# Optimization experiments

Measured on AMD Instinct MI355X. Metric: run time of the kernel, lower is better.

## Reference

```python
import jax, jax.numpy as jnp
import numpy as np

B, S, I, H = 128, 1024, 512, 1024


def setup_inputs() -> dict:
    key = jax.random.key(0)
    k0, k1, k2 = jax.random.split(key, 3)
    scale = 0.02
    return {
        "x": jax.random.normal(k0, (B, S, I), jnp.float32),
        "feature_weighting": jnp.ones((1, 1, I), jnp.float32),
        "temporal_weighting": jnp.ones((1, S, 1), jnp.float32),
        "magnitude": jnp.ones((1,), jnp.float32),
        "W0": jax.random.normal(k1, (3 * H, I + H), jnp.float32) * scale,
        "b0": jnp.zeros((3 * H,), jnp.float32),
        "W1": jax.random.normal(k2, (3 * H, 2 * H), jnp.float32) * scale,
        "b1": jnp.zeros((3 * H,), jnp.float32),
    }


def _cell(x_t, h_prev, c_prev, W, b):
    # gates: [B, 3H] from cat(x, h_prev) @ W.T + b
    gates = jnp.concatenate([x_t, h_prev], axis=1) @ W.T + b
    i, g, o = jnp.split(gates, 3, axis=1)
    f = jax.nn.sigmoid(c_prev)            # note: forget gate from c_prev (module's quirk)
    c_new = f * c_prev + jax.nn.sigmoid(i) * jnp.tanh(g)
    h_new = jax.nn.sigmoid(o) * jnp.tanh(c_new) * f  # extra *f (module's quirk)
    return h_new, c_new


def reference(x, feature_weighting, temporal_weighting, magnitude, W0, b0, W1, b1):
    batch = x.shape[0]
    hid = W0.shape[0] // 3
    x = x * feature_weighting * temporal_weighting * jnp.exp(magnitude)
    zeros = jnp.zeros((batch, hid), x.dtype)
    init = (zeros, zeros, zeros, zeros)  # h0, c0, h1, c1

    def step(carry, x_t):
        h0, c0, h1, c1 = carry
        h0, c0 = _cell(x_t, h0, c0, W0, b0)
        h1, c1 = _cell(h0, h1, c1, W1, b1)
        return (h0, c0, h1, c1), h1

    (h0, c0, h1, c1), ys = jax.lax.scan(step, init, jnp.swapaxes(x, 0, 1))
    outputs = jnp.swapaxes(ys, 0, 1)  # [B, S, H]
    return outputs, ((h0, c0), (h1, c1))
```

## Files before the change

kernel.cpp:

```cpp
#include <hip/hip_runtime.h>
#include <hip/hip_bf16.h>


typedef __attribute__((ext_vector_type(8))) _Float16 f16x8;
typedef __attribute__((ext_vector_type(4))) float f32x4;
typedef unsigned long long u64;
#define DEV __device__ __forceinline__

namespace {
constexpr int Bb = 128, Ss = 1024, Ii = 512, Hh = 1024;
constexpr int K0 = Ii + Hh;
constexpr int K1 = 2 * Hh;
constexpr int NWG = 256;
constexpr int NPH = Ss + 1;
constexpr int RING = 16;

constexpr size_t BH    = (size_t)Bb * Hh;
constexpr size_t OF_H0 = (size_t)Bb * Ss * Hh;
constexpr size_t OF_C0 = OF_H0 + BH;
constexpr size_t OF_H1 = OF_C0 + BH;
constexpr size_t OF_C1 = OF_H1 + BH;

constexpr size_t WS_GO    = 0;
constexpr size_t WS_SLOTS = 256;
constexpr size_t WS_C0    = 4096;
constexpr size_t WS_C1    = WS_C0 + BH * 4;
constexpr size_t RINGF    = (size_t)RING * BH * 2;
constexpr size_t WS_H0F   = WS_C1 + BH * 4;
constexpr size_t WS_H1F   = WS_H0F + RINGF;
constexpr size_t WS_ZEND  = WS_H1F + RINGF;
constexpr size_t WSZ_W0   = (size_t)3 * Hh * K0 * 2;
constexpr size_t WSZ_W1   = (size_t)3 * Hh * K1 * 2;
constexpr size_t WS_W0F   = WS_ZEND;
constexpr size_t WS_W1F   = WS_W0F + WSZ_W0;
constexpr size_t WS_NEED  = WS_W1F + WSZ_W1;

constexpr int CHUNKB    = 3072;
constexpr int LO_BYTES  = 48 * CHUNKB;
constexpr int RED_BYTES = 4 * 3 * 64 * 16;
constexpr int DYN_LDS   = LO_BYTES + RED_BYTES;
}

DEV unsigned short f16b(float f) {
  return __builtin_bit_cast(unsigned short, (_Float16)f);
}
DEV float sig_(float x) { return 1.f / (1.f + __expf(-x)); }
DEV float tanh_(float x) {
  float e = __expf(-2.f * fabsf(x));
  return copysignf((1.f - e) / (1.f + e), x);
}
DEV f16x8 ldh(const unsigned short* p) { return *reinterpret_cast<const f16x8*>(p); }
#define MFMAH __builtin_amdgcn_mfma_f32_16x16x32_f16

__global__ void k_zero(uint4* p, int n16) {
  for (int i = blockIdx.x * blockDim.x + threadIdx.x; i < n16; i += gridDim.x * blockDim.x)
    p[i] = make_uint4(0u, 0u, 0u, 0u);
}

__global__ void k_convert(const float* __restrict__ W0, const float* __restrict__ W1,
                          unsigned short* __restrict__ w0f, unsigned short* __restrict__ w1f) {
  const long NW04 = (long)3 * Hh * K0 / 4;
  const long NW14 = (long)3 * Hh * K1 / 4;
  const long total = NW04 + NW14;
  for (long i = (long)blockIdx.x * blockDim.x + threadIdx.x; i < total;
       i += (long)gridDim.x * blockDim.x) {
    long e; const float* src; unsigned short* dst;
    if (i < NW04) { e = i * 4;          src = W0 + e; dst = w0f + e; }
    else          { e = (i - NW04) * 4; src = W1 + e; dst = w1f + e; }
    f32x4 v = *(const f32x4*)src;
    u64 pk = 0;
#pragma unroll
    for (int e2 = 0; e2 < 4; ++e2) pk |= (u64)f16b(v[e2]) << (16 * e2);
    *(u64*)dst = pk;
  }
}

#define LD_W(g, kl)                                                           \
  (*(const f16x8*)(lds + ((kl) >> 5) * CHUNKB + (g) * 1024 + l4 * 256 + l15 * 16))

#define BLOCK8_L(hP, kaB, koB)                                                \
  do {                                                                        \
    f16x8 aH[8];                                                              \
    _Pragma("unroll") for (int c8 = 0; c8 < 8; ++c8)                          \
      aH[c8] = ldh((hP) + (kaB) + c8 * 32);                                   \
    _Pragma("unroll") for (int c8 = 0; c8 < 8; ++c8) {                        \
      const int ko_ = (koB) + c8 * 32;                                        \
      f32x4 &I = (c8 & 1) ? aI1 : aI0;                                        \
      f32x4 &G = (c8 & 1) ? aG1 : aG0;                                        \
      f32x4 &O = (c8 & 1) ? aO1 : aO0;                                        \
      I = MFMAH(LD_W(0, ko_), aH[c8], I, 0, 0, 0);                            \
      G = MFMAH(LD_W(1, ko_), aH[c8], G, 0, 0, 0);                            \
      O = MFMAH(LD_W(2, ko_), aH[c8], O, 0, 0, 0);                            \
    }                                                                         \
  } while (0)

#define BLOCK4_G(hP, kaB, koB)                                                \
  do {                                                                        \
    f16x8 aH[4], wA[4], wB[4], wC[4];                                         \
    _Pragma("unroll") for (int c4 = 0; c4 < 4; ++c4) {                        \
      const int ko_ = (koB) + c4 * 32, ka_ = (kaB) + c4 * 32;                 \
      wA[c4] = ldh(wf + off0 + ko_);                                          \
      wB[c4] = ldh(wf + off1 + ko_);                                          \
      wC[c4] = ldh(wf + off2 + ko_);                                          \
      aH[c4] = ldh((hP) + ka_);                                               \
    }                                                                         \
    _Pragma("unroll") for (int c4 = 0; c4 < 4; ++c4) {                        \
      f32x4 &I = (c4 & 1) ? aI1 : aI0;                                        \
      f32x4 &G = (c4 & 1) ? aG1 : aG0;                                        \
      f32x4 &O = (c4 & 1) ? aO1 : aO0;                                        \
      I = MFMAH(wA[c4], aH[c4], I, 0, 0, 0);                                  \
      G = MFMAH(wB[c4], aH[c4], G, 0, 0, 0);                                  \
      O = MFMAH(wC[c4], aH[c4], O, 0, 0, 0);                                  \
    }                                                                         \
  } while (0)

#define BLOCK4_X(pxP, kB)                                                     \
  do {                                                                        \
    f32x4 x0_[4], x1_[4], f0_[4], f1_[4];                                     \
    _Pragma("unroll") for (int c4 = 0; c4 < 4; ++c4) {                        \
      const int k_ = (kB) + c4 * 32;                                          \
      x0_[c4] = *(const f32x4*)((pxP) + k_);                                  \
      x1_[c4] = *(const f32x4*)((pxP) + k_ + 4);                              \
      f0_[c4] = *(const f32x4*)(fw + k_ + l4 * 8);                            \
      f1_[c4] = *(const f32x4*)(fw + k_ + l4 * 8 + 4);                        \
    }                                                                         \
    _Pragma("unroll") for (int c4 = 0; c4 < 4; ++c4) {                        \
      const int k_ = (kB) + c4 * 32;                                          \
      f32x4 xs0 = x0_[c4] * f0_[c4] * twm, xs1 = x1_[c4] * f1_[c4] * twm;     \
      f16x8 a;                                                                \
      _Pragma("unroll") for (int e = 0; e < 4; ++e) {                         \
        a[e] = (_Float16)xs0[e];                                              \
        a[e + 4] = (_Float16)xs1[e];                                          \
      }                                                                       \
      f32x4 &I = (c4 & 1) ? aI1 : aI0;                                        \
      f32x4 &G = (c4 & 1) ? aG1 : aG0;                                        \
      f32x4 &O = (c4 & 1) ? aO1 : aO0;                                        \
      I = MFMAH(LD_W(0, k_), a, I, 0, 0, 0);                                  \
      G = MFMAH(LD_W(1, k_), a, G, 0, 0, 0);                                  \
      O = MFMAH(LD_W(2, k_), a, O, 0, 0, 0);                                  \
    }                                                                         \
  } while (0)

__global__ __launch_bounds__(512, 2) void lstm_persist(
    const float* __restrict__ xf,
    const float* __restrict__ fw, const float* __restrict__ tw, const float* __restrict__ mag,
    const unsigned short* __restrict__ w0f, const float* __restrict__ b0,
    const unsigned short* __restrict__ w1f, const float* __restrict__ b1,
    float* __restrict__ out,
    unsigned short* __restrict__ h0f, unsigned short* __restrict__ h1f,
    float* __restrict__ c0, float* __restrict__ c1,
    int* __restrict__ slots, int* __restrict__ go) {
  extern __shared__ char lds[];
  f32x4* red = reinterpret_cast<f32x4*>(lds + LO_BYTES);

  const int tid = threadIdx.x;
  const int lane = tid & 63;
  const int wv = tid >> 6;
  const int mt = wv & 3;
  const int kh = wv >> 2;
  const int l15 = lane & 15, l4 = lane >> 4;

  const int wg = blockIdx.x;
  const int layer = wg >> 7;
  const int i = wg & 127;
  const int x8 = i & 7, kk = i >> 3;
  const int jt = x8 * 8 + (kk >> 1);
  const int mg = kk & 1;
  const int jb = jt * 16;

  const int bact = mg * 64 + mt * 16 + l15;
  const int j0 = jb + l4 * 4;

  const int K = layer ? K1 : K0;
  const unsigned short* wf = layer ? w1f : w0f;
  const size_t off0 = (size_t)(0 * Hh + jb + l15) * K + l4 * 8;
  const size_t off1 = (size_t)(1 * Hh + jb + l15) * K + l4 * 8;
  const size_t off2 = (size_t)(2 * Hh + jb + l15) * K + l4 * 8;

  const float* bb = layer ? b1 : b0;
  const f32x4 bi = *(const f32x4*)(bb + j0);
  const f32x4 bg = *(const f32x4*)(bb + Hh + j0);
  const f32x4 bo = *(const f32x4*)(bb + 2 * Hh + j0);

  float* cst = (layer ? c1 : c0) + (size_t)bact * Hh + j0;
  float* outb = out + (size_t)bact * Ss * Hh + j0;
  const float emag = __expf(mag[0]);

  {
    const u64* wsl = (const u64*)wf;
    const int K4 = K >> 2;
    for (int idx = tid; idx < 48 * 384; idx += 512) {
      int R = idx / 384;
      int o = idx - R * 384;
      int g = R >> 4, rr = R & 15;
      u64 v = wsl[(size_t)(g * Hh + jb + rr) * K4 + o];
      *(u64*)(lds + (o >> 3) * CHUNKB + g * 1024 + ((o >> 1) & 3) * 256 +
              rr * 16 + (o & 1) * 8) = v;
    }
  }
  __syncthreads();

  for (int p = 0; p < NPH; ++p) {
    const bool act = layer ? (p >= 1) : (p < Ss);
    const int t = layer ? (p - 1) : p;
    const int rslot = (p - 1) & (RING - 1);
    const int wslot = p & (RING - 1);

    if (act) {
      f32x4 z = {0.f, 0.f, 0.f, 0.f};
      f32x4 aI0 = z, aG0 = z, aO0 = z, aI1 = z, aG1 = z, aO1 = z;
      const unsigned short* h0r = h0f + (size_t)rslot * BH + (size_t)bact * Hh + l4 * 8;
      const unsigned short* h1r = h1f + (size_t)rslot * BH + (size_t)bact * Hh + l4 * 8;

      if (layer == 0) {
        if (kh == 0) {
          const float* px = xf + ((size_t)bact * Ss + t) * Ii + l4 * 8;
          const float twm = tw[t] * emag;
          BLOCK4_X(px, 0);
          BLOCK4_X(px, 128);
          BLOCK4_X(px, 256);
          BLOCK4_X(px, 384);
          BLOCK8_L(h0r, 0, Ii);
        } else {
          BLOCK8_L(h0r, 256, Ii + 256);
          BLOCK8_L(h0r, 512, Ii + 512);
          BLOCK8_L(h0r, 768, Ii + 768);
        }
      } else {
        if (kh == 0) {
          BLOCK8_L(h0r, 0, 0);
          BLOCK8_L(h0r, 256, 256);
          BLOCK8_L(h0r, 512, 512);
          BLOCK8_L(h0r, 768, 768);
        } else {
          BLOCK8_L(h1r, 0, Hh);
          BLOCK8_L(h1r, 256, Hh + 256);
          BLOCK4_G(h1r, 512, Hh + 512);
          BLOCK4_G(h1r, 640, Hh + 640);
          BLOCK4_G(h1r, 768, Hh + 768);
          BLOCK4_G(h1r, 896, Hh + 896);
        }
      }

      if (kh == 1) {
        red[((mt * 3 + 0) << 6) + lane] = aI0 + aI1;
        red[((mt * 3 + 1) << 6) + lane] = aG0 + aG1;
        red[((mt * 3 + 2) << 6) + lane] = aO0 + aO1;
      }
      __syncthreads();
      if (kh == 0) {
        f32x4 ai = aI0 + aI1 + red[((mt * 3 + 0) << 6) + lane] + bi;
        f32x4 ag = aG0 + aG1 + red[((mt * 3 + 1) << 6) + lane] + bg;
        f32x4 ao = aO0 + aO1 + red[((mt * 3 + 2) << 6) + lane] + bo;
        f32x4 cp = *(const f32x4*)cst;
        f32x4 cn, hn;
        u64 hpk = 0;
#pragma unroll
        for (int r = 0; r < 4; ++r) {
          float f = sig_(cp[r]);
          float cc = f * cp[r] + sig_(ai[r]) * tanh_(ag[r]);
          float hh = sig_(ao[r]) * tanh_(cc) * f;
          cn[r] = cc; hn[r] = hh;
          hpk |= (u64)f16b(hh) << (16 * r);
        }
        *(f32x4*)cst = cn;
        const size_t wbase = (size_t)wslot * BH + (size_t)bact * Hh + j0;
        __hip_atomic_store((u64*)((layer ? h1f : h0f) + wbase), hpk,
                           __ATOMIC_RELAXED, __HIP_MEMORY_SCOPE_AGENT);
        if (layer) {
          *(f32x4*)(outb + (size_t)t * Hh) = hn;
          if (t == Ss - 1) {
            *(f32x4*)(out + OF_H1 + (size_t)bact * Hh + j0) = hn;
            *(f32x4*)(out + OF_C1 + (size_t)bact * Hh + j0) = cn;
          }
        } else if (t == Ss - 1) {
          *(f32x4*)(out + OF_H0 + (size_t)bact * Hh + j0) = hn;
          *(f32x4*)(out + OF_C0 + (size_t)bact * Hh + j0) = cn;
        }
      }
    }

    if (p < NPH - 1) {
      __syncthreads();
      if (wg == 0) {
        if (tid == 0)
          __hip_atomic_store(&slots[0], p + 1, __ATOMIC_RELAXED, __HIP_MEMORY_SCOPE_AGENT);
        int gd = 0; bool ok;
        do {
          ok = true;
          if (tid < 256)
            ok = __hip_atomic_load(&slots[tid], __ATOMIC_RELAXED, __HIP_MEMORY_SCOPE_AGENT) > p;
          if (!ok) __builtin_amdgcn_s_sleep(1);
        } while (!__syncthreads_and(ok) && ++gd < (1 << 22));
        if (tid == 0)
          __hip_atomic_store(go, p + 1, __ATOMIC_RELAXED, __HIP_MEMORY_SCOPE_AGENT);
      } else {
        if (tid == 0) {
          __hip_atomic_store(&slots[wg], p + 1, __ATOMIC_RELAXED, __HIP_MEMORY_SCOPE_AGENT);
          int gd = 0;
          while (__hip_atomic_load(go, __ATOMIC_RELAXED, __HIP_MEMORY_SCOPE_AGENT) <= p &&
                 ++gd < (1 << 24))
            __builtin_amdgcn_s_sleep(1);
        }
        __syncthreads();
      }
      if ((p & (RING - 1)) == (RING - 1)) {
        if (tid == 0) __builtin_amdgcn_fence(__ATOMIC_ACQUIRE, "agent");
        __syncthreads();
      }
    }
  }
}

extern "C" void kernel_launch(void* const* d_in, const int* in_sizes, int n_in,
                              void* d_out, int out_size, void* d_ws, size_t ws_size,
                              hipStream_t stream) {
  const float* x   = (const float*)d_in[0];
  const float* fw  = (const float*)d_in[1];
  const float* tw  = (const float*)d_in[2];
  const float* mag = (const float*)d_in[3];
  const float* W0  = (const float*)d_in[4];
  const float* b0  = (const float*)d_in[5];
  const float* W1  = (const float*)d_in[6];
  const float* b1  = (const float*)d_in[7];
  float* out = (float*)d_out;
  char* ws = (char*)d_ws;

  if (ws_size < WS_NEED) return;

  unsigned short* w0f = (unsigned short*)(ws + WS_W0F);
  unsigned short* w1f = (unsigned short*)(ws + WS_W1F);

  (void)hipFuncSetAttribute((const void*)lstm_persist,
                            hipFuncAttributeMaxDynamicSharedMemorySize, DYN_LDS);

  k_zero<<<2320, 256, 0, stream>>>((uint4*)ws, (int)(WS_ZEND / 16));
  k_convert<<<1024, 256, 0, stream>>>(W0, W1, w0f, w1f);

  lstm_persist<<<NWG, 512, DYN_LDS, stream>>>(
      x, fw, tw, mag, w0f, b0, w1f, b1, out,
      (unsigned short*)(ws + WS_H0F), (unsigned short*)(ws + WS_H1F),
      (float*)(ws + WS_C0), (float*)(ws + WS_C1),
      (int*)(ws + WS_SLOTS), (int*)(ws + WS_GO));
}
```

Baseline: 15.90 ms.

## Rebalance K split, prefetch x, pad barrier slots, shrink ring, remap workgroups

Several changes land together. Barrier slot and go flags are padded to separate cache lines, and the go flag is replicated eight ways so waiters poll different addresses, which reduces contention in the grid barrier. The input x for the next timestep is loaded, scaled and converted ahead of time into registers, overlapping that global load with the barrier wait. The K split between the two half-warps is rebalanced and the h loads are issued in larger batches, and the workgroup-to-tile mapping and ring depth are changed. The cost is higher register pressure from the larger prefetch and h arrays, plus more frequent acquire fences now that the ring is smaller.

After: 16.93 ms. +6.5%, slower.

```diff
diff --git a/kernel.cpp b/kernel.cpp
--- a/kernel.cpp
+++ b/kernel.cpp
@@ -13,7 +13,8 @@
 constexpr int K1 = 2 * Hh;
 constexpr int NWG = 256;
 constexpr int NPH = Ss + 1;
-constexpr int RING = 16;
+constexpr int RING = 8;
+constexpr int SSTR = 32;
 
 constexpr size_t BH    = (size_t)Bb * Hh;
 constexpr size_t OF_H0 = (size_t)Bb * Ss * Hh;
@@ -22,8 +23,8 @@
 constexpr size_t OF_C1 = OF_H1 + BH;
 
 constexpr size_t WS_GO    = 0;
-constexpr size_t WS_SLOTS = 256;
-constexpr size_t WS_C0    = 4096;
+constexpr size_t WS_SLOTS = 4096;
+constexpr size_t WS_C0    = 40960;
 constexpr size_t WS_C1    = WS_C0 + BH * 4;
 constexpr size_t RINGF    = (size_t)RING * BH * 2;
 constexpr size_t WS_H0F   = WS_C1 + BH * 4;
@@ -78,66 +79,65 @@
 #define LD_W(g, kl)                                                           \
   (*(const f16x8*)(lds + ((kl) >> 5) * CHUNKB + (g) * 1024 + l4 * 256 + l15 * 16))
 
-#define BLOCK8_L(hP, kaB, koB)                                                \
+#define HLOAD(arr, n, hP, kaB)                                                \
+  _Pragma("unroll") for (int c_ = 0; c_ < (n); ++c_)                          \
+    arr[c_] = ldh((hP) + (kaB) + c_ * 32);
+
+#define HCOMP(arr, n, koB)                                                    \
+  _Pragma("unroll") for (int c_ = 0; c_ < (n); ++c_) {                        \
+    const int ko_ = (koB) + c_ * 32;                                          \
+    f32x4 &I_ = (c_ & 1) ? aI1 : aI0;                                         \
+    f32x4 &G_ = (c_ & 1) ? aG1 : aG0;                                         \
+    f32x4 &O_ = (c_ & 1) ? aO1 : aO0;                                         \
+    I_ = MFMAH(LD_W(0, ko_), arr[c_], I_, 0, 0, 0);                           \
+    G_ = MFMAH(LD_W(1, ko_), arr[c_], G_, 0, 0, 0);                           \
+    O_ = MFMAH(LD_W(2, ko_), arr[c_], O_, 0, 0, 0);                           \
+  }
+
+#define WLOAD(a0, a1, a2, n, koB)                                             \
+  _Pragma("unroll") for (int c_ = 0; c_ < (n); ++c_) {                        \
+    const int ko_ = (koB) + c_ * 32;                                          \
+    a0[c_] = ldh(wf + off0 + ko_);                                            \
+    a1[c_] = ldh(wf + off1 + ko_);                                            \
+    a2[c_] = ldh(wf + off2 + ko_);                                            \
+  }
+
+#define GCOMP(h_, a0, a1, a2, n)                                              \
+  _Pragma("unroll") for (int c_ = 0; c_ < (n); ++c_) {                        \
+    f32x4 &I_ = (c_ & 1) ? aI1 : aI0;                                         \
+    f32x4 &G_ = (c_ & 1) ? aG1 : aG0;                                         \
+    f32x4 &O_ = (c_ & 1) ? aO1 : aO0;                                         \
+    I_ = MFMAH(a0[c_], h_[c_], I_, 0, 0, 0);                                  \
+    G_ = MFMAH(a1[c_], h_[c_], G_, 0, 0, 0);                                  \
+    O_ = MFMAH(a2[c_], h_[c_], O_, 0, 0, 0);                                  \
+  }
+
+#define XCOMP()                                                               \
+  _Pragma("unroll") for (int c_ = 0; c_ < 16; ++c_) {                         \
+    const int ko_ = c_ * 32;                                                  \
+    f32x4 &I_ = (c_ & 1) ? aI1 : aI0;                                         \
+    f32x4 &G_ = (c_ & 1) ? aG1 : aG0;                                         \
+    f32x4 &O_ = (c_ & 1) ? aO1 : aO0;                                         \
+    I_ = MFMAH(LD_W(0, ko_), xp[c_], I_, 0, 0, 0);                            \
+    G_ = MFMAH(LD_W(1, ko_), xp[c_], G_, 0, 0, 0);                            \
+    O_ = MFMAH(LD_W(2, ko_), xp[c_], O_, 0, 0, 0);                            \
+  }
+
+#define XPREF(tn)                                                             \
   do {                                                                        \
-    f16x8 aH[8];                                                              \
-    _Pragma("unroll") for (int c8 = 0; c8 < 8; ++c8)                          \
-      aH[c8] = ldh((hP) + (kaB) + c8 * 32);                                   \
-    _Pragma("unroll") for (int c8 = 0; c8 < 8; ++c8) {                        \
-      const int ko_ = (koB) + c8 * 32;                                        \
-      f32x4 &I = (c8 & 1) ? aI1 : aI0;                                        \
-      f32x4 &G = (c8 & 1) ? aG1 : aG0;                                        \
-      f32x4 &O = (c8 & 1) ? aO1 : aO0;                                        \
-      I = MFMAH(LD_W(0, ko_), aH[c8], I, 0, 0, 0);                            \
-      G = MFMAH(LD_W(1, ko_), aH[c8], G, 0, 0, 0);                            \
-      O = MFMAH(LD_W(2, ko_), aH[c8], O, 0, 0, 0);                            \
-    }                                                                         \
-  } while (0)
-
-#define BLOCK4_G(hP, kaB, koB)                                                \
-  do {                                                                        \
-    f16x8 aH[4], wA[4], wB[4], wC[4];                                         \
-    _Pragma("unroll") for (int c4 = 0; c4 < 4; ++c4) {                        \
-      const int ko_ = (koB) + c4 * 32, ka_ = (kaB) + c4 * 32;                 \
-      wA[c4] = ldh(wf + off0 + ko_);                                          \
-      wB[c4] = ldh(wf + off1 + ko_);                                          \
-      wC[c4] = ldh(wf + off2 + ko_);                                          \
-      aH[c4] = ldh((hP) + ka_);                                               \
-    }                                                                         \
-    _Pragma("unroll") for (int c4 = 0; c4 < 4; ++c4) {                        \
-      f32x4 &I = (c4 & 1) ? aI1 : aI0;                                        \
-      f32x4 &G = (c4 & 1) ? aG1 : aG0;                                        \
-      f32x4 &O = (c4 & 1) ? aO1 : aO0;                                        \
-      I = MFMAH(wA[c4], aH[c4], I, 0, 0, 0);                                  \
-      G = MFMAH(wB[c4], aH[c4], G, 0, 0, 0);                                  \
-      O = MFMAH(wC[c4], aH[c4], O, 0, 0, 0);                                  \
-    }                                                                         \
-  } while (0)
-
-#define BLOCK4_X(pxP, kB)                                                     \
-  do {                                                                        \
-    f32x4 x0_[4], x1_[4], f0_[4], f1_[4];                                     \
-    _Pragma("unroll") for (int c4 = 0; c4 < 4; ++c4) {                        \
-      const int k_ = (kB) + c4 * 32;                                          \
-      x0_[c4] = *(const f32x4*)((pxP) + k_);                                  \
-      x1_[c4] = *(const f32x4*)((pxP) + k_ + 4);                              \
-      f0_[c4] = *(const f32x4*)(fw + k_ + l4 * 8);                            \
-      f1_[c4] = *(const f32x4*)(fw + k_ + l4 * 8 + 4);                        \
-    }                                                                         \
-    _Pragma("unroll") for (int c4 = 0; c4 < 4; ++c4) {                        \
-      const int k_ = (kB) + c4 * 32;                                          \
-      f32x4 xs0 = x0_[c4] * f0_[c4] * twm, xs1 = x1_[c4] * f1_[c4] * twm;     \
-      f16x8 a;                                                                \
-      _Pragma("unroll") for (int e = 0; e < 4; ++e) {                         \
-        a[e] = (_Float16)xs0[e];                                              \
-        a[e + 4] = (_Float16)xs1[e];                                          \
+    const float* pxn_ = xf + ((size_t)bact * Ss + (tn)) * Ii + l4 * 8;        \
+    const float twn_ = tw[tn] * emag;                                         \
+    _Pragma("unroll") for (int c_ = 0; c_ < 16; ++c_) {                       \
+      const int k_ = c_ * 32;                                                 \
+      f32x4 a0_ = *(const f32x4*)(pxn_ + k_);                                 \
+      f32x4 a1_ = *(const f32x4*)(pxn_ + k_ + 4);                             \
+      f32x4 b0_ = *(const f32x4*)(fw + k_ + l4 * 8);                          \
+      f32x4 b1_ = *(const f32x4*)(fw + k_ + l4 * 8 + 4);                      \
+      a0_ *= b0_ * twn_; a1_ *= b1_ * twn_;                                   \
+      _Pragma("unroll") for (int e_ = 0; e_ < 4; ++e_) {                      \
+        xp[c_][e_] = (_Float16)a0_[e_];                                       \
+        xp[c_][e_ + 4] = (_Float16)a1_[e_];                                   \
       }                                                                       \
-      f32x4 &I = (c4 & 1) ? aI1 : aI0;                                        \
-      f32x4 &G = (c4 & 1) ? aG1 : aG0;                                        \
-      f32x4 &O = (c4 & 1) ? aO1 : aO0;                                        \
-      I = MFMAH(LD_W(0, k_), a, I, 0, 0, 0);                                  \
-      G = MFMAH(LD_W(1, k_), a, G, 0, 0, 0);                                  \
-      O = MFMAH(LD_W(2, k_), a, O, 0, 0, 0);                                  \
     }                                                                         \
   } while (0)
 
@@ -163,9 +163,10 @@
   const int wg = blockIdx.x;
   const int layer = wg >> 7;
   const int i = wg & 127;
-  const int x8 = i & 7, kk = i >> 3;
-  const int jt = x8 * 8 + (kk >> 1);
-  const int mg = kk & 1;
+  const int x8 = i & 7;
+  const int kk = i >> 3;
+  const int mg = x8 >> 2;
+  const int jt = (x8 & 3) * 16 + kk;
   const int jb = jt * 16;
 
   const int bact = mg * 64 + mt * 16 + l15;
@@ -198,6 +199,8 @@
               rr * 16 + (o & 1) * 8) = v;
     }
   }
+  f16x8 xp[16];
+  if (layer == 0 && kh == 0) XPREF(0);
   __syncthreads();
 
   for (int p = 0; p < NPH; ++p) {
@@ -214,31 +217,49 @@
 
       if (layer == 0) {
         if (kh == 0) {
-          const float* px = xf + ((size_t)bact * Ss + t) * Ii + l4 * 8;
-          const float twm = tw[t] * emag;
-          BLOCK4_X(px, 0);
-          BLOCK4_X(px, 128);
-          BLOCK4_X(px, 256);
-          BLOCK4_X(px, 384);
-          BLOCK8_L(h0r, 0, Ii);
+          f16x8 hA[12];
+          HLOAD(hA, 12, h0r, 0);
+          XCOMP();
+          HCOMP(hA, 12, Ii);
         } else {
-          BLOCK8_L(h0r, 256, Ii + 256);
-          BLOCK8_L(h0r, 512, Ii + 512);
-          BLOCK8_L(h0r, 768, Ii + 768);
+          f16x8 hA[10], hB[10];
+          HLOAD(hA, 10, h0r, 384);
+          HLOAD(hB, 10, h0r, 704);
+          HCOMP(hA, 10, Ii + 384);
+          HCOMP(hB, 10, Ii + 704);
         }
       } else {
         if (kh == 0) {
-          BLOCK8_L(h0r, 0, 0);
-          BLOCK8_L(h0r, 256, 256);
-          BLOCK8_L(h0r, 512, 512);
-          BLOCK8_L(h0r, 768, 768);
+          f16x8 g0[12], g1[12], g2a[8], g2b[4], g3[12];
+          HLOAD(g0, 12, h0r, 0);
+          HLOAD(g1, 12, h0r, 384);
+          HCOMP(g0, 12, 0);
+          HLOAD(g2a, 8, h0r, 768);
+          HLOAD(g2b, 4, h1r, 0);
+          HCOMP(g1, 12, 384);
+          HLOAD(g3, 12, h1r, 128);
+          HCOMP(g2a, 8, 768);
+          HCOMP(g2b, 4, Hh);
+          HCOMP(g3, 12, Hh + 128);
         } else {
-          BLOCK8_L(h1r, 0, Hh);
-          BLOCK8_L(h1r, 256, Hh + 256);
-          BLOCK4_G(h1r, 512, Hh + 512);
-          BLOCK4_G(h1r, 640, Hh + 640);
-          BLOCK4_G(h1r, 768, Hh + 768);
-          BLOCK4_G(h1r, 896, Hh + 896);
+          {
+            f16x8 sh[6], sA[6], sB[6], sC[6];
+            HLOAD(sh, 6, h1r, 512);
+            WLOAD(sA, sB, sC, 6, Hh + 512);
+            GCOMP(sh, sA, sB, sC, 6);
+          }
+          {
+            f16x8 sh[6], sA[6], sB[6], sC[6];
+            HLOAD(sh, 6, h1r, 704);
+            WLOAD(sA, sB, sC, 6, Hh + 704);
+            GCOMP(sh, sA, sB, sC, 6);
+          }
+          {
+            f16x8 sh[4], sA[4], sB[4], sC[4];
+            HLOAD(sh, 4, h1r, 896);
+            WLOAD(sA, sB, sC, 4, Hh + 896);
+            GCOMP(sh, sA, sB, sC, 4);
+          }
         }
       }
 
@@ -278,6 +299,7 @@
           *(f32x4*)(out + OF_C0 + (size_t)bact * Hh + j0) = cn;
         }
       }
+      if (layer == 0 && kh == 0 && t + 1 < Ss) XPREF(t + 1);
     }
 
     if (p < NPH - 1) {
@@ -289,16 +311,20 @@
         do {
           ok = true;
           if (tid < 256)
-            ok = __hip_atomic_load(&slots[tid], __ATOMIC_RELAXED, __HIP_MEMORY_SCOPE_AGENT) > p;
+            ok = __hip_atomic_load(&slots[tid * SSTR], __ATOMIC_RELAXED,
+                                   __HIP_MEMORY_SCOPE_AGENT) > p;
           if (!ok) __builtin_amdgcn_s_sleep(1);
         } while (!__syncthreads_and(ok) && ++gd < (1 << 22));
-        if (tid == 0)
-          __hip_atomic_store(go, p + 1, __ATOMIC_RELAXED, __HIP_MEMORY_SCOPE_AGENT);
+        if (tid < 8)
+          __hip_atomic_store(&go[tid * SSTR], p + 1, __ATOMIC_RELAXED,
+                             __HIP_MEMORY_SCOPE_AGENT);
       } else {
         if (tid == 0) {
-          __hip_atomic_store(&slots[wg], p + 1, __ATOMIC_RELAXED, __HIP_MEMORY_SCOPE_AGENT);
+          __hip_atomic_store(&slots[wg * SSTR], p + 1, __ATOMIC_RELAXED,
+                             __HIP_MEMORY_SCOPE_AGENT);
           int gd = 0;
-          while (__hip_atomic_load(go, __ATOMIC_RELAXED, __HIP_MEMORY_SCOPE_AGENT) <= p &&
+          while (__hip_atomic_load(&go[x8 * SSTR], __ATOMIC_RELAXED,
+                                   __HIP_MEMORY_SCOPE_AGENT) <= p &&
                  ++gd < (1 << 24))
             __builtin_amdgcn_s_sleep(1);
         }
@@ -334,7 +360,7 @@
   (void)hipFuncSetAttribute((const void*)lstm_persist,
                             hipFuncAttributeMaxDynamicSharedMemorySize, DYN_LDS);
 
-  k_zero<<<2320, 256, 0, stream>>>((uint4*)ws, (int)(WS_ZEND / 16));
+  k_zero<<<1290, 256, 0, stream>>>((uint4*)ws, (int)(WS_ZEND / 16));
   k_convert<<<1024, 256, 0, stream>>>(W0, W1, w0f, w1f);
 
   lstm_persist<<<NWG, 512, DYN_LDS, stream>>>(
```
